# Performance work log

Hardware: AMD Instinct MI355X
Metric: run time of the kernel (lower is better)

## Reference

```python
import jax, jax.numpy as jnp
import numpy as np

STEPS = 30
BATCH = 1048576
HIDDEN = 32


def setup_inputs() -> dict:
    key = jax.random.key(0)
    k_s, k_w1, k_b1, k_w2, k_b2 = jax.random.split(key, 5)
    return {
        "S": jax.random.normal(k_s, (BATCH, STEPS), dtype=jnp.float32),
        "W1": jax.random.normal(k_w1, (3, HIDDEN), dtype=jnp.float32) * (1.0 / np.sqrt(3.0)),
        "b1": jax.random.normal(k_b1, (HIDDEN,), dtype=jnp.float32) * 0.01,
        "W2": jax.random.normal(k_w2, (HIDDEN, 1), dtype=jnp.float32) * (1.0 / np.sqrt(HIDDEN)),
        "b2": jax.random.normal(k_b2, (1,), dtype=jnp.float32) * 0.01,
        "a_init": jnp.zeros((1,), dtype=jnp.float32),
    }


def reference(S, W1, b1, W2, b2, a_init):
    B = S.shape[0]
    h0 = jnp.zeros((B, 1), dtype=S.dtype)
    d0 = jnp.broadcast_to(a_init.reshape(1, 1), (B, 1))  # a_init.expand(batch, 1)

    def step(carry, s_t):
        h, d_prev = carry
        x = jnp.concatenate([s_t[:, None], d_prev, h], axis=1)  # (B, 3)
        hidden = jax.nn.relu(x @ W1 + b1)                        # (B, 32)
        d = hidden @ W2 + b2                                     # (B, 1)
        h_new = 0.8 * h + 0.2 * d
        return (h_new, d), d

    # scan over time: S.T has shape (steps, B)
    (_, _), deltas = jax.lax.scan(step, (h0, d0), S.T)
    # deltas: (steps, B, 1) -> (B, steps)
    return jnp.transpose(deltas[:, :, 0], (1, 0))
```

## Files before the change

### kernel.cpp

```cpp
#include <hip/hip_runtime.h>

#define STEPS 30
#define HID 32
#define TPB 256
#define EPB 128
#define LDS_STRIDE (STEPS + 1)

typedef float f32x16 __attribute__((ext_vector_type(16)));
typedef __fp16 h8 __attribute__((ext_vector_type(8)));
typedef unsigned int u32x4 __attribute__((ext_vector_type(4)));

static __device__ __forceinline__ unsigned int pkrtz_u32(float x, float y) {
    return __builtin_bit_cast(unsigned int, __builtin_amdgcn_cvt_pkrtz(x, y));
}

__global__ __launch_bounds__(TPB, 4) void hedge_kernel(
    const float* __restrict__ S,
    const float* __restrict__ W1,
    const float* __restrict__ b1,
    const float* __restrict__ W2,
    const float* __restrict__ b2,
    const float* __restrict__ a_init,
    float* __restrict__ out)
{
    __shared__ float tile[EPB * LDS_STRIDE];
    const int tid  = threadIdx.x;
    const int lane = tid & 63;
    const int wv   = tid >> 6;
    const long long base = (long long)blockIdx.x * (EPB * STEPS);

    #pragma unroll
    for (int k = 0; k < (EPB * STEPS) / TPB; ++k) {
        int idx = tid + k * TPB;
        float v = S[base + idx];
        int row = idx / STEPS;
        int col = idx - row * STEPS;
        tile[row * LDS_STRIDE + col] = v;
    }

    const int j = lane & 31;
    const float wbf = b1[j];
    const float waf = W1[0 * HID + j];
    const float wcf = W1[1 * HID + j];
    const float wef = W1[2 * HID + j];
    u32x4 av;
    if (lane < 32) {
        av[0] = pkrtz_u32(wbf, waf);
        av[1] = pkrtz_u32(wcf, wef);
        av[2] = 0u; av[3] = 0u;
    } else {
        av[0] = 0u; av[1] = 0u; av[2] = 0u; av[3] = 0u;
    }
    const h8 afrag = __builtin_bit_cast(h8, av);

    const int rbase = 4 * (lane >> 5);
    float w2r[16];
    #pragma unroll
    for (int r = 0; r < 16; ++r)
        w2r[r] = W2[(r & 3) + 8 * (r >> 2) + rbase];

    const float bias2 = b2[0];
    float d = a_init[0];
    float h = 0.0f;
    const f32x16 zero16 = {0.f};
    __syncthreads();

    float* my = &tile[(32 * wv + (lane & 31)) * LDS_STRIDE];
    #pragma unroll
    for (int t = 0; t < STEPS; ++t) {
        const float s = my[t];
        u32x4 bv;
        bv[0] = pkrtz_u32(1.0f, s);
        bv[1] = pkrtz_u32(d, h);
        bv[2] = bv[0]; bv[3] = bv[1];
        const h8 bfrag = __builtin_bit_cast(h8, bv);

        const f32x16 P = __builtin_amdgcn_mfma_f32_32x32x16_f16(afrag, bfrag, zero16, 0, 0, 0);

        float a0 = 0.f, a1 = 0.f, a2 = 0.f, a3 = 0.f;
        #pragma unroll
        for (int r = 0; r < 16; r += 4) {
            a0 = fmaf(w2r[r + 0], fmaxf(P[r + 0], 0.f), a0);
            a1 = fmaf(w2r[r + 1], fmaxf(P[r + 1], 0.f), a1);
            a2 = fmaf(w2r[r + 2], fmaxf(P[r + 2], 0.f), a2);
            a3 = fmaf(w2r[r + 3], fmaxf(P[r + 3], 0.f), a3);
        }
        float part = (a0 + a1) + (a2 + a3);
        part += __shfl_xor(part, 32);
        const float dn = bias2 + part;
        h = fmaf(0.2f, dn, 0.8f * h);
        d = dn;
        my[t] = dn;
    }
    __syncthreads();

    #pragma unroll
    for (int k = 0; k < (EPB * STEPS) / TPB; ++k) {
        int idx = tid + k * TPB;
        int row = idx / STEPS;
        int col = idx - row * STEPS;
        out[base + idx] = tile[row * LDS_STRIDE + col];
    }
}

extern "C" void kernel_launch(void* const* d_in, const int* in_sizes, int n_in,
                              void* d_out, int out_size, void* d_ws, size_t ws_size,
                              hipStream_t stream) {
    const float* S      = (const float*)d_in[0];
    const float* W1     = (const float*)d_in[1];
    const float* b1     = (const float*)d_in[2];
    const float* W2     = (const float*)d_in[3];
    const float* b2     = (const float*)d_in[4];
    const float* a_init = (const float*)d_in[5];
    float* out = (float*)d_out;

    const int batch = in_sizes[0] / STEPS;
    const int grid  = batch / EPB;
    hedge_kernel<<<grid, TPB, 0, stream>>>(S, W1, b1, W2, b2, a_init, out);
}
```

Measured before the change: 259.6 us.

## Process two batch elements per lane with interleaved MFMA chains and vectorized IO

```diff
diff --git a/kernel.cpp b/kernel.cpp
--- a/kernel.cpp
+++ b/kernel.cpp
@@ -3,7 +3,7 @@
 #define STEPS 30
 #define HID 32
 #define TPB 256
-#define EPB 128
+#define EPB 256
 #define LDS_STRIDE (STEPS + 1)
 
 typedef float f32x16 __attribute__((ext_vector_type(16)));
@@ -29,13 +29,15 @@
     const int wv   = tid >> 6;
     const long long base = (long long)blockIdx.x * (EPB * STEPS);
 
+    const float2* S2 = (const float2*)(S + base);
     #pragma unroll
-    for (int k = 0; k < (EPB * STEPS) / TPB; ++k) {
-        int idx = tid + k * TPB;
-        float v = S[base + idx];
-        int row = idx / STEPS;
-        int col = idx - row * STEPS;
-        tile[row * LDS_STRIDE + col] = v;
+    for (int k = 0; k < (EPB * STEPS) / (2 * TPB); ++k) {
+        int i2 = tid + k * TPB;
+        float2 v = S2[i2];
+        int row = i2 / 15;
+        int col = 2 * (i2 - row * 15);
+        float* p = &tile[row * LDS_STRIDE + col];
+        p[0] = v.x; p[1] = v.y;
     }
 
     const int j = lane & 31;
@@ -60,46 +62,66 @@
         w2r[r] = W2[(r & 3) + 8 * (r >> 2) + rbase];
 
     const float bias2 = b2[0];
-    float d = a_init[0];
-    float h = 0.0f;
+    const float d_init = a_init[0];
+    float dA = d_init, hA = 0.0f;
+    float dB = d_init, hB = 0.0f;
     const f32x16 zero16 = {0.f};
     __syncthreads();
 
-    float* my = &tile[(32 * wv + (lane & 31)) * LDS_STRIDE];
+    const int erow = 64 * wv + (lane & 31);
+    float* myA = &tile[erow * LDS_STRIDE];
+    float* myB = &tile[(erow + 32) * LDS_STRIDE];
     #pragma unroll
     for (int t = 0; t < STEPS; ++t) {
-        const float s = my[t];
-        u32x4 bv;
-        bv[0] = pkrtz_u32(1.0f, s);
-        bv[1] = pkrtz_u32(d, h);
-        bv[2] = bv[0]; bv[3] = bv[1];
-        const h8 bfrag = __builtin_bit_cast(h8, bv);
+        const float sA = myA[t];
+        const float sB = myB[t];
 
-        const f32x16 P = __builtin_amdgcn_mfma_f32_32x32x16_f16(afrag, bfrag, zero16, 0, 0, 0);
+        u32x4 bvA, bvB;
+        bvA[0] = pkrtz_u32(1.0f, sA);
+        bvA[1] = pkrtz_u32(dA, hA);
+        bvA[2] = bvA[0]; bvA[3] = bvA[1];
+        bvB[0] = pkrtz_u32(1.0f, sB);
+        bvB[1] = pkrtz_u32(dB, hB);
+        bvB[2] = bvB[0]; bvB[3] = bvB[1];
 
-        float a0 = 0.f, a1 = 0.f, a2 = 0.f, a3 = 0.f;
+        const f32x16 PA = __builtin_amdgcn_mfma_f32_32x32x16_f16(
+            afrag, __builtin_bit_cast(h8, bvA), zero16, 0, 0, 0);
+        const f32x16 PB = __builtin_amdgcn_mfma_f32_32x32x16_f16(
+            afrag, __builtin_bit_cast(h8, bvB), zero16, 0, 0, 0);
+
+        float a0 = 0.f, a1 = 0.f, b0 = 0.f, b1v = 0.f;
         #pragma unroll
-        for (int r = 0; r < 16; r += 4) {
-            a0 = fmaf(w2r[r + 0], fmaxf(P[r + 0], 0.f), a0);
-            a1 = fmaf(w2r[r + 1], fmaxf(P[r + 1], 0.f), a1);
-            a2 = fmaf(w2r[r + 2], fmaxf(P[r + 2], 0.f), a2);
-            a3 = fmaf(w2r[r + 3], fmaxf(P[r + 3], 0.f), a3);
+        for (int r = 0; r < 16; r += 2) {
+            a0  = fmaf(w2r[r + 0], fmaxf(PA[r + 0], 0.f), a0);
+            a1  = fmaf(w2r[r + 1], fmaxf(PA[r + 1], 0.f), a1);
+            b0  = fmaf(w2r[r + 0], fmaxf(PB[r + 0], 0.f), b0);
+            b1v = fmaf(w2r[r + 1], fmaxf(PB[r + 1], 0.f), b1v);
         }
-        float part = (a0 + a1) + (a2 + a3);
-        part += __shfl_xor(part, 32);
-        const float dn = bias2 + part;
-        h = fmaf(0.2f, dn, 0.8f * h);
-        d = dn;
-        my[t] = dn;
+        float partA = a0 + a1;
+        float partB = b0 + b1v;
+        partA += __shfl_xor(partA, 32);
+        partB += __shfl_xor(partB, 32);
+        const float dnA = bias2 + partA;
+        const float dnB = bias2 + partB;
+        hA = fmaf(0.2f, dnA, 0.8f * hA);
+        hB = fmaf(0.2f, dnB, 0.8f * hB);
+        dA = dnA;
+        dB = dnB;
+        if (lane < 32) {
+            myA[t] = dnA;
+            myB[t] = dnB;
+        }
     }
     __syncthreads();
 
+    float2* O2 = (float2*)(out + base);
     #pragma unroll
-    for (int k = 0; k < (EPB * STEPS) / TPB; ++k) {
-        int idx = tid + k * TPB;
-        int row = idx / STEPS;
-        int col = idx - row * STEPS;
-        out[base + idx] = tile[row * LDS_STRIDE + col];
+    for (int k = 0; k < (EPB * STEPS) / (2 * TPB); ++k) {
+        int i2 = tid + k * TPB;
+        int row = i2 / 15;
+        int col = 2 * (i2 - row * 15);
+        const float* p = &tile[row * LDS_STRIDE + col];
+        O2[i2] = make_float2(p[0], p[1]);
     }
 }
 
```

Measured after the change: 252.9 us. 2.6% less time.
